# Kernel tuning notes

Hardware: AMD Instinct MI355X
Metric: run time of the kernel (lower is better)

The kernel has to match this reference:

```python
import jax, jax.numpy as jnp
import numpy as np
from jax import lax

SEQ, B, IN, H, L = 1024, 128, 256, 512, 2


def _brc_layer(x_seq, h0, Uc, wc, bc, Ua, wa, ba, Uh, bh):
    # Precompute the input projections for all timesteps (big batched matmuls),
    # then scan the purely elementwise BRC recurrence over time.
    pc = jnp.einsum('tbi,hi->tbh', x_seq, Uc) + bc  # [T,B,H]
    pa = jnp.einsum('tbi,hi->tbh', x_seq, Ua) + ba
    ph = jnp.einsum('tbi,hi->tbh', x_seq, Uh) + bh

    def step(h, proj):
        pc_t, pa_t, ph_t = proj
        c = jax.nn.sigmoid(pc_t + wc * h)
        a = 1.0 + jnp.tanh(pa_t + wa * h)
        h = c * h + (1.0 - c) * jnp.tanh(ph_t + a * h)
        return h, h

    hn, y_seq = lax.scan(step, h0, (pc, pa, ph))
    return y_seq, hn


def setup_inputs() -> dict:
    key = jax.random.key(0)
    ks = jax.random.split(key, 20)

    def xavier(k, shape):
        fan_in, fan_out = shape[1], shape[0]
        s = jnp.sqrt(6.0 / (fan_in + fan_out)).astype(jnp.float32)
        return jax.random.uniform(k, shape, jnp.float32, -s, s)

    return {
        'x_seq': jax.random.normal(ks[0], (SEQ, B, IN), jnp.float32),
        'h0': jnp.zeros((L, B, H), jnp.float32),
        'Uc0': xavier(ks[1], (H, IN)),
        'wc0': jax.random.normal(ks[2], (H,), jnp.float32),
        'bc0': jax.random.normal(ks[3], (H,), jnp.float32),
        'Ua0': xavier(ks[4], (H, IN)),
        'wa0': jax.random.normal(ks[5], (H,), jnp.float32),
        'ba0': jax.random.normal(ks[6], (H,), jnp.float32),
        'Uh0': xavier(ks[7], (H, IN)),
        'bh0': jax.random.normal(ks[8], (H,), jnp.float32),
        'Uc1': xavier(ks[9], (H, H)),
        'wc1': jax.random.normal(ks[10], (H,), jnp.float32),
        'bc1': jax.random.normal(ks[11], (H,), jnp.float32),
        'Ua1': xavier(ks[12], (H, H)),
        'wa1': jax.random.normal(ks[13], (H,), jnp.float32),
        'ba1': jax.random.normal(ks[14], (H,), jnp.float32),
        'Uh1': xavier(ks[15], (H, H)),
        'bh1': jax.random.normal(ks[16], (H,), jnp.float32),
    }


def reference(x_seq, h0, Uc0, wc0, bc0, Ua0, wa0, ba0, Uh0, bh0,
              Uc1, wc1, bc1, Ua1, wa1, ba1, Uh1, bh1):
    y0, hn0 = _brc_layer(x_seq, h0[0], Uc0, wc0, bc0, Ua0, wa0, ba0, Uh0, bh0)
    y1, hn1 = _brc_layer(y0, h0[1], Uc1, wc1, bc1, Ua1, wa1, ba1, Uh1, bh1)
    hn = jnp.stack([hn0, hn1], axis=0)  # [L,B,H]
    return y1, hn
```

## Files before the change

### kernel.cpp

```cpp
#include <hip/hip_runtime.h>
#include <cstdint>
#include <cstddef>

typedef _Float16 f16;
typedef _Float16 f16x4 __attribute__((ext_vector_type(4)));
typedef _Float16 f16x8 __attribute__((ext_vector_type(8)));
typedef float f32x4 __attribute__((ext_vector_type(4)));

#define SEQ 1024
#define BATCH 128
#define INDIM 256
#define HDIM 512
#define MROWS (SEQ * BATCH)
#define NCOLS (3 * HDIM)
#define BHDIM (BATCH * HDIM)
#define TCHUNK 256
#define CHROWS (TCHUNK * BATCH)
#define NCH (SEQ / TCHUNK)

#define P32_OFF   0ull
#define Y0_OFF    201326592ull
#define WHI_OFF   469762048ull
#define WLO_OFF   471334912ull
#define BIAS_OFF  472907776ull
#define HST_OFF   472913920ull
#define WS_NEEDED 473176064ull

__device__ __forceinline__ float fast_tanh(float x) {
  return 1.0f - 2.0f / (__expf(2.0f * x) + 1.0f);
}
__device__ __forceinline__ float fast_sigmoid(float x) {
  return 1.0f / (1.0f + __expf(-x));
}

__device__ __forceinline__ void split4(const float* __restrict__ in, f16* __restrict__ hi,
                                       f16* __restrict__ lo, int i) {
  float4 v = reinterpret_cast<const float4*>(in)[i];
  f16x4 h4 = {(f16)v.x, (f16)v.y, (f16)v.z, (f16)v.w};
  f16x4 l4 = {(f16)((v.x - (float)h4[0]) * 2048.0f),
              (f16)((v.y - (float)h4[1]) * 2048.0f),
              (f16)((v.z - (float)h4[2]) * 2048.0f),
              (f16)((v.w - (float)h4[3]) * 2048.0f)};
  reinterpret_cast<f16x4*>(hi)[i] = h4;
  reinterpret_cast<f16x4*>(lo)[i] = l4;
}

__global__ __launch_bounds__(256) void prep_kernel(
    const float* __restrict__ w0, const float* __restrict__ w1, const float* __restrict__ w2,
    f16* __restrict__ wh, f16* __restrict__ wl, int n4w,
    const float* __restrict__ b0, const float* __restrict__ b1, const float* __restrict__ b2,
    float* __restrict__ bias, int nb4) {
  const int total = 3 * n4w + 3 * nb4;
  const int stride = gridDim.x * blockDim.x;
  for (int i = blockIdx.x * blockDim.x + threadIdx.x; i < total; i += stride) {
    if (i < 3 * n4w) {
      int m = i / n4w;
      int off = i - m * n4w;
      const float* src = (m == 0) ? w0 : ((m == 1) ? w1 : w2);
      split4(src, wh + (long)m * n4w * 4, wl + (long)m * n4w * 4, off);
    } else {
      int k = i - 3 * n4w;
      int m = k / nb4;
      int off = k - m * nb4;
      const float* src = (m == 0) ? b0 : ((m == 1) ? b1 : b2);
      reinterpret_cast<float4*>(bias)[m * nb4 + off] =
          reinterpret_cast<const float4*>(src)[off];
    }
  }
}

__global__ __launch_bounds__(256, 2) void gemm_split_kernel(
    const float* __restrict__ A,
    const f16* __restrict__ Whi, const f16* __restrict__ Wlo,
    const float* __restrict__ bias, float* __restrict__ P, int K) {
  constexpr int BK = 32;
  constexpr int LDSS = BK + 8;
  __shared__ f16 sAh[2][128 * LDSS];
  __shared__ f16 sAl[2][128 * LDSS];
  __shared__ f16 sBh[2][128 * LDSS];
  __shared__ f16 sBl[2][128 * LDSS];

  const int tid = threadIdx.x;
  const int lane = tid & 63;
  const int w = tid >> 6;
  const int wm = (w >> 1) * 64;
  const int wn = (w & 1) * 64;

  const int per = gridDim.x >> 3;
  const int logical = (blockIdx.x & 7) * per + (blockIdx.x >> 3);
  const int nb = logical % (NCOLS / 128);
  const int mb = logical / (NCOLS / 128);
  const long m0 = (long)mb * 128;
  const int n0 = nb * 128;

  const int fr = lane & 15;
  const int fk = (lane >> 4) * 8;

  const int arow = tid >> 3;
  const int ac4 = (tid & 7) << 2;
  const int brow = tid >> 2;
  const int bc8 = (tid & 3) << 3;

  f32x4 acc[4][4] = {};
  f32x4 accc[4][4] = {};

  const int NT = K / BK;

  float4 rA[4];
  f16x8 rBh[2], rBl[2];

#define LOADR(tt)                                                              \
  do {                                                                         \
    const int k0 = (tt) * BK;                                                  \
    _Pragma("unroll")                                                          \
    for (int r = 0; r < 4; ++r)                                                \
      rA[r] = *reinterpret_cast<const float4*>(A + (m0 + r * 32 + arow) * (long)K + k0 + ac4); \
    _Pragma("unroll")                                                          \
    for (int r = 0; r < 2; ++r) {                                              \
      const long gb = (n0 + r * 64 + brow) * (long)K + k0 + bc8;               \
      rBh[r] = *reinterpret_cast<const f16x8*>(Whi + gb);                      \
      rBl[r] = *reinterpret_cast<const f16x8*>(Wlo + gb);                      \
    }                                                                          \
  } while (0)
#define WRITEB(buf)                                                            \
  do {                                                                         \
    _Pragma("unroll")                                                          \
    for (int r = 0; r < 4; ++r) {                                              \
      f16x4 h4 = {(f16)rA[r].x, (f16)rA[r].y, (f16)rA[r].z, (f16)rA[r].w};     \
      f16x4 l4 = {(f16)((rA[r].x - (float)h4[0]) * 2048.0f),                   \
                  (f16)((rA[r].y - (float)h4[1]) * 2048.0f),                   \
                  (f16)((rA[r].z - (float)h4[2]) * 2048.0f),                   \
                  (f16)((rA[r].w - (float)h4[3]) * 2048.0f)};                  \
      *reinterpret_cast<f16x4*>(&sAh[(buf)][(r * 32 + arow) * LDSS + ac4]) = h4; \
      *reinterpret_cast<f16x4*>(&sAl[(buf)][(r * 32 + arow) * LDSS + ac4]) = l4; \
    }                                                                          \
    _Pragma("unroll")                                                          \
    for (int r = 0; r < 2; ++r) {                                              \
      *reinterpret_cast<f16x8*>(&sBh[(buf)][(r * 64 + brow) * LDSS + bc8]) = rBh[r]; \
      *reinterpret_cast<f16x8*>(&sBl[(buf)][(r * 64 + brow) * LDSS + bc8]) = rBl[r]; \
    }                                                                          \
  } while (0)

  LOADR(0);
  WRITEB(0);
  __syncthreads();

  int cur = 0;
  for (int t = 0; t < NT; ++t) {
    const bool pf = (t + 1) < NT;
    if (pf) LOADR(t + 1);

    f16x8 ah[4], al[4], bh[4], bl[4];
#pragma unroll
    for (int i = 0; i < 4; ++i) {
      ah[i] = *reinterpret_cast<const f16x8*>(&sAh[cur][(wm + i * 16 + fr) * LDSS + fk]);
      al[i] = *reinterpret_cast<const f16x8*>(&sAl[cur][(wm + i * 16 + fr) * LDSS + fk]);
      bh[i] = *reinterpret_cast<const f16x8*>(&sBh[cur][(wn + i * 16 + fr) * LDSS + fk]);
      bl[i] = *reinterpret_cast<const f16x8*>(&sBl[cur][(wn + i * 16 + fr) * LDSS + fk]);
    }

    __builtin_amdgcn_s_setprio(1);
#pragma unroll
    for (int i = 0; i < 4; ++i)
#pragma unroll
      for (int j = 0; j < 4; ++j) {
        acc[i][j]  = __builtin_amdgcn_mfma_f32_16x16x32_f16(ah[i], bh[j], acc[i][j], 0, 0, 0);
        accc[i][j] = __builtin_amdgcn_mfma_f32_16x16x32_f16(ah[i], bl[j], accc[i][j], 0, 0, 0);
        accc[i][j] = __builtin_amdgcn_mfma_f32_16x16x32_f16(al[i], bh[j], accc[i][j], 0, 0, 0);
      }
    __builtin_amdgcn_s_setprio(0);

    if (pf) {
      WRITEB(cur ^ 1);
      __syncthreads();
      cur ^= 1;
    }
  }
#undef LOADR
#undef WRITEB

  const int crow = (lane >> 4) * 4;
  const int ccol = lane & 15;
#pragma unroll
  for (int j = 0; j < 4; ++j) {
    int gc = n0 + wn + j * 16 + ccol;
    float bv = bias[gc];
#pragma unroll
    for (int i = 0; i < 4; ++i) {
      long gr = m0 + wm + i * 16 + crow;
#pragma unroll
      for (int r = 0; r < 4; ++r) {
        P[(gr + r) * NCOLS + gc] = acc[i][j][r] + accc[i][j][r] * (1.0f / 2048.0f) + bv;
      }
    }
  }
}

__global__ __launch_bounds__(256) void scan_kernel(
    const float* __restrict__ P, const float* __restrict__ hinit,
    float* __restrict__ hstate, int first,
    const float* __restrict__ wc, const float* __restrict__ wa,
    float* __restrict__ Y, float* __restrict__ HN) {
  const int j = blockIdx.x * 256 + threadIdx.x;
  const int hh = j & (HDIM - 1);
  float h = first ? hinit[j] : hstate[j];
  const float wcv = wc[hh];
  const float wav = wa[hh];
  const float* p = P + (long)(j >> 9) * NCOLS + hh;
  float* y = Y + j;
#pragma unroll 4
  for (int t = 0; t < TCHUNK; ++t) {
    float pc = p[0];
    float pa = p[HDIM];
    float ph = p[2 * HDIM];
    float c = fast_sigmoid(fmaf(wcv, h, pc));
    float a = 1.0f + fast_tanh(fmaf(wav, h, pa));
    h = c * h + (1.0f - c) * fast_tanh(fmaf(a, h, ph));
    *y = h;
    y += BHDIM;
    p += BATCH * NCOLS;
  }
  hstate[j] = h;
  if (HN) HN[j] = h;
}

extern "C" void kernel_launch(void* const* d_in, const int* in_sizes, int n_in,
                              void* d_out, int out_size, void* d_ws, size_t ws_size,
                              hipStream_t stream) {
  const float* x   = (const float*)d_in[0];
  const float* h0  = (const float*)d_in[1];
  const float* Uc0 = (const float*)d_in[2];
  const float* wc0 = (const float*)d_in[3];
  const float* bc0 = (const float*)d_in[4];
  const float* Ua0 = (const float*)d_in[5];
  const float* wa0 = (const float*)d_in[6];
  const float* ba0 = (const float*)d_in[7];
  const float* Uh0 = (const float*)d_in[8];
  const float* bh0 = (const float*)d_in[9];
  const float* Uc1 = (const float*)d_in[10];
  const float* wc1 = (const float*)d_in[11];
  const float* bc1 = (const float*)d_in[12];
  const float* Ua1 = (const float*)d_in[13];
  const float* wa1 = (const float*)d_in[14];
  const float* ba1 = (const float*)d_in[15];
  const float* Uh1 = (const float*)d_in[16];
  const float* bh1 = (const float*)d_in[17];

  if (ws_size < WS_NEEDED) return;

  char* ws = (char*)d_ws;
  float* p32  = (float*)(ws + P32_OFF);
  float* y0   = (float*)(ws + Y0_OFF);
  f16* whi    = (f16*)(ws + WHI_OFF);
  f16* wlo    = (f16*)(ws + WLO_OFF);
  float* bias = (float*)(ws + BIAS_OFF);
  float* hst  = (float*)(ws + HST_OFF);

  float* y1  = (float*)d_out;
  float* hn0 = y1 + (long)SEQ * BHDIM;
  float* hn1 = hn0 + BHDIM;

  const dim3 gemm_grid((CHROWS / 128) * (NCOLS / 128));

  hipLaunchKernelGGL(prep_kernel, dim3(512), dim3(256), 0, stream,
                     Uc0, Ua0, Uh0, whi, wlo, HDIM * INDIM / 4,
                     bc0, ba0, bh0, bias, HDIM / 4);

  for (int tc = 0; tc < NCH; ++tc) {
    hipLaunchKernelGGL(gemm_split_kernel, gemm_grid, dim3(256), 0, stream,
                       x + (long)tc * CHROWS * INDIM, whi, wlo, bias, p32, INDIM);
    hipLaunchKernelGGL(scan_kernel, dim3(BHDIM / 256), dim3(256), 0, stream,
                       p32, h0, hst, (tc == 0) ? 1 : 0, wc0, wa0,
                       y0 + (long)tc * TCHUNK * BHDIM,
                       (tc == NCH - 1) ? hn0 : (float*)nullptr);
  }

  hipLaunchKernelGGL(prep_kernel, dim3(512), dim3(256), 0, stream,
                     Uc1, Ua1, Uh1, whi, wlo, HDIM * HDIM / 4,
                     bc1, ba1, bh1, bias, HDIM / 4);

  for (int tc = 0; tc < NCH; ++tc) {
    hipLaunchKernelGGL(gemm_split_kernel, gemm_grid, dim3(256), 0, stream,
                       y0 + (long)tc * CHROWS * HDIM, whi, wlo, bias, p32, HDIM);
    hipLaunchKernelGGL(scan_kernel, dim3(BHDIM / 256), dim3(256), 0, stream,
                       p32, h0 + BHDIM, hst, (tc == 0) ? 1 : 0, wc1, wa1,
                       y1 + (long)tc * TCHUNK * BHDIM,
                       (tc == NCH - 1) ? hn1 : (float*)nullptr);
  }
}
```

Measured before the change: 1.624 ms.

## Store GEMM LDS tiles in MFMA fragment order for contiguous lane reads

Measured after the change: 1.852 ms. 14.0% more time.

```diff
diff --git a/kernel.cpp b/kernel.cpp
--- a/kernel.cpp
+++ b/kernel.cpp
@@ -74,17 +74,18 @@
     const f16* __restrict__ Whi, const f16* __restrict__ Wlo,
     const float* __restrict__ bias, float* __restrict__ P, int K) {
   constexpr int BK = 32;
-  constexpr int LDSS = BK + 8;
-  __shared__ f16 sAh[2][128 * LDSS];
-  __shared__ f16 sAl[2][128 * LDSS];
-  __shared__ f16 sBh[2][128 * LDSS];
-  __shared__ f16 sBl[2][128 * LDSS];
+  __shared__ f16 sAh[2][4096];
+  __shared__ f16 sAl[2][4096];
+  __shared__ f16 sBh[2][4096];
+  __shared__ f16 sBl[2][4096];
 
   const int tid = threadIdx.x;
   const int lane = tid & 63;
   const int w = tid >> 6;
   const int wm = (w >> 1) * 64;
   const int wn = (w & 1) * 64;
+  const int wmg = wm >> 4;
+  const int wng = wn >> 4;
 
   const int per = gridDim.x >> 3;
   const int logical = (blockIdx.x & 7) * per + (blockIdx.x >> 3);
@@ -93,52 +94,59 @@
   const long m0 = (long)mb * 128;
   const int n0 = nb * 128;
 
-  const int fr = lane & 15;
-  const int fk = (lane >> 4) * 8;
-
-  const int arow = tid >> 3;
-  const int ac4 = (tid & 7) << 2;
-  const int brow = tid >> 2;
-  const int bc8 = (tid & 3) << 3;
+  const int u0 = tid, u1 = tid + 256;
+  const int r0w = (u0 >> 6) * 16 + (u0 & 15), k0w = ((u0 >> 4) & 3) * 8;
+  const int r1w = (u1 >> 6) * 16 + (u1 & 15), k1w = ((u1 >> 4) & 3) * 8;
+  const long ga0 = (m0 + r0w) * (long)K + k0w;
+  const long ga1 = (m0 + r1w) * (long)K + k1w;
+  const long gb0 = (n0 + r0w) * (long)K + k0w;
+  const long gb1 = (n0 + r1w) * (long)K + k1w;
+  const int l0 = u0 * 8, l1 = u1 * 8;
+  const int lb = lane * 8;
 
   f32x4 acc[4][4] = {};
   f32x4 accc[4][4] = {};
 
   const int NT = K / BK;
 
-  float4 rA[4];
-  f16x8 rBh[2], rBl[2];
+  float4 rA0a, rA0b, rA1a, rA1b;
+  f16x8 rBh0, rBh1, rBl0, rBl1;
 
 #define LOADR(tt)                                                              \
   do {                                                                         \
     const int k0 = (tt) * BK;                                                  \
-    _Pragma("unroll")                                                          \
-    for (int r = 0; r < 4; ++r)                                                \
-      rA[r] = *reinterpret_cast<const float4*>(A + (m0 + r * 32 + arow) * (long)K + k0 + ac4); \
-    _Pragma("unroll")                                                          \
-    for (int r = 0; r < 2; ++r) {                                              \
-      const long gb = (n0 + r * 64 + brow) * (long)K + k0 + bc8;               \
-      rBh[r] = *reinterpret_cast<const f16x8*>(Whi + gb);                      \
-      rBl[r] = *reinterpret_cast<const f16x8*>(Wlo + gb);                      \
-    }                                                                          \
+    rA0a = *reinterpret_cast<const float4*>(A + ga0 + k0);                     \
+    rA0b = *reinterpret_cast<const float4*>(A + ga0 + k0 + 4);                 \
+    rA1a = *reinterpret_cast<const float4*>(A + ga1 + k0);                     \
+    rA1b = *reinterpret_cast<const float4*>(A + ga1 + k0 + 4);                 \
+    rBh0 = *reinterpret_cast<const f16x8*>(Whi + gb0 + k0);                    \
+    rBh1 = *reinterpret_cast<const f16x8*>(Whi + gb1 + k0);                    \
+    rBl0 = *reinterpret_cast<const f16x8*>(Wlo + gb0 + k0);                    \
+    rBl1 = *reinterpret_cast<const f16x8*>(Wlo + gb1 + k0);                    \
   } while (0)
+#define SPLIT8(va, vb, h8, l8)                                                 \
+  f16x8 h8 = {(f16)va.x, (f16)va.y, (f16)va.z, (f16)va.w,                      \
+              (f16)vb.x, (f16)vb.y, (f16)vb.z, (f16)vb.w};                     \
+  f16x8 l8 = {(f16)((va.x - (float)h8[0]) * 2048.0f),                          \
+              (f16)((va.y - (float)h8[1]) * 2048.0f),                          \
+              (f16)((va.z - (float)h8[2]) * 2048.0f),                          \
+              (f16)((va.w - (float)h8[3]) * 2048.0f),                          \
+              (f16)((vb.x - (float)h8[4]) * 2048.0f),                          \
+              (f16)((vb.y - (float)h8[5]) * 2048.0f),                          \
+              (f16)((vb.z - (float)h8[6]) * 2048.0f),                          \
+              (f16)((vb.w - (float)h8[7]) * 2048.0f)}
 #define WRITEB(buf)                                                            \
   do {                                                                         \
-    _Pragma("unroll")                                                          \
-    for (int r = 0; r < 4; ++r) {                                              \
-      f16x4 h4 = {(f16)rA[r].x, (f16)rA[r].y, (f16)rA[r].z, (f16)rA[r].w};     \
-      f16x4 l4 = {(f16)((rA[r].x - (float)h4[0]) * 2048.0f),                   \
-                  (f16)((rA[r].y - (float)h4[1]) * 2048.0f),                   \
-                  (f16)((rA[r].z - (float)h4[2]) * 2048.0f),                   \
-                  (f16)((rA[r].w - (float)h4[3]) * 2048.0f)};                  \
-      *reinterpret_cast<f16x4*>(&sAh[(buf)][(r * 32 + arow) * LDSS + ac4]) = h4; \
-      *reinterpret_cast<f16x4*>(&sAl[(buf)][(r * 32 + arow) * LDSS + ac4]) = l4; \
-    }                                                                          \
-    _Pragma("unroll")                                                          \
-    for (int r = 0; r < 2; ++r) {                                              \
-      *reinterpret_cast<f16x8*>(&sBh[(buf)][(r * 64 + brow) * LDSS + bc8]) = rBh[r]; \
-      *reinterpret_cast<f16x8*>(&sBl[(buf)][(r * 64 + brow) * LDSS + bc8]) = rBl[r]; \
-    }                                                                          \
+    SPLIT8(rA0a, rA0b, h80, l80);                                              \
+    SPLIT8(rA1a, rA1b, h81, l81);                                              \
+    *reinterpret_cast<f16x8*>(&sAh[(buf)][l0]) = h80;                          \
+    *reinterpret_cast<f16x8*>(&sAl[(buf)][l0]) = l80;                          \
+    *reinterpret_cast<f16x8*>(&sAh[(buf)][l1]) = h81;                          \
+    *reinterpret_cast<f16x8*>(&sAl[(buf)][l1]) = l81;                          \
+    *reinterpret_cast<f16x8*>(&sBh[(buf)][l0]) = rBh0;                         \
+    *reinterpret_cast<f16x8*>(&sBh[(buf)][l1]) = rBh1;                         \
+    *reinterpret_cast<f16x8*>(&sBl[(buf)][l0]) = rBl0;                         \
+    *reinterpret_cast<f16x8*>(&sBl[(buf)][l1]) = rBl1;                         \
   } while (0)
 
   LOADR(0);
@@ -153,10 +161,10 @@
     f16x8 ah[4], al[4], bh[4], bl[4];
 #pragma unroll
     for (int i = 0; i < 4; ++i) {
-      ah[i] = *reinterpret_cast<const f16x8*>(&sAh[cur][(wm + i * 16 + fr) * LDSS + fk]);
-      al[i] = *reinterpret_cast<const f16x8*>(&sAl[cur][(wm + i * 16 + fr) * LDSS + fk]);
-      bh[i] = *reinterpret_cast<const f16x8*>(&sBh[cur][(wn + i * 16 + fr) * LDSS + fk]);
-      bl[i] = *reinterpret_cast<const f16x8*>(&sBl[cur][(wn + i * 16 + fr) * LDSS + fk]);
+      ah[i] = *reinterpret_cast<const f16x8*>(&sAh[cur][(wmg + i) * 512 + lb]);
+      al[i] = *reinterpret_cast<const f16x8*>(&sAl[cur][(wmg + i) * 512 + lb]);
+      bh[i] = *reinterpret_cast<const f16x8*>(&sBh[cur][(wng + i) * 512 + lb]);
+      bl[i] = *reinterpret_cast<const f16x8*>(&sBl[cur][(wng + i) * 512 + lb]);
     }
 
     __builtin_amdgcn_s_setprio(1);
@@ -177,6 +185,7 @@
     }
   }
 #undef LOADR
+#undef SPLIT8
 #undef WRITEB
 
   const int crow = (lane >> 4) * 4;
```
